# Optimization experiments

Measured on AMD Instinct MI355X. Metric: run time of the kernel, lower is better.

Reference implementation:

```python
import jax, jax.numpy as jnp
import numpy as np

B, IN, OUT, ORDER = 8192, 1024, 1024, 7


def setup_inputs() -> dict:
    key = jax.random.key(0)
    k1, k2 = jax.random.split(key)
    x = jax.random.normal(k1, (B, IN), dtype=jnp.float32)
    tanh_range = jnp.float32(1.0)
    coef = jax.random.normal(k2, (OUT, IN, ORDER + 1), dtype=jnp.float32) * 0.1
    return {"x": x, "tanh_range": tanh_range, "coef": coef}


def _poly(x, tanh_range, order):
    # t^0, t^1, ..., t^order via cumulative products (matches torch recurrence)
    t = jnp.tanh(x * tanh_range)                      # [B, IN]
    powers = jnp.cumprod(jnp.broadcast_to(t[..., None], t.shape + (order,)), axis=-1)
    ones = jnp.ones_like(t)[..., None]
    return jnp.concatenate([ones, powers], axis=-1)   # [B, IN, order+1]


def reference(x, tanh_range, coef):
    poly = _poly(x, tanh_range, ORDER)                # [B, IN, K]
    # output[b, j] = sum_{i,k} coef[j,i,k] * poly[b,i,k]
    return jnp.einsum('bik,jik->bj', poly, coef)
```

## Files before the change

kernel.cpp:

```cpp
#include <hip/hip_runtime.h>
#include <hip/hip_bf16.h>


#define BM 128
#define BN 128
#define BK 64
#define KT 7168
#define KFULL 8192

typedef short bf16x8 __attribute__((ext_vector_type(8)));
typedef short bf16x4 __attribute__((ext_vector_type(4)));
typedef float f32x4  __attribute__((ext_vector_type(4)));

__device__ __forceinline__ unsigned short f2bf(float f) {
    union { float f; unsigned u; } v; v.f = f;
    unsigned r = v.u + 0x7fffu + ((v.u >> 16) & 1u);
    return (unsigned short)(r >> 16);
}

__device__ __forceinline__ void gload_lds16(const void* gp, void* lp) {
    __builtin_amdgcn_global_load_lds(
        (const __attribute__((address_space(1))) void*)gp,
        (__attribute__((address_space(3))) void*)lp, 16, 0, 0);
}

#define CVT_BLOCKS  512
#define TANH_BLOCKS 4096

__global__ __launch_bounds__(256)
void prep(const float* __restrict__ x, const float* __restrict__ trp,
          const float* __restrict__ coef, unsigned short* __restrict__ coef_bf,
          unsigned short* __restrict__ A) {
    const int b = blockIdx.x;
    unsigned short tmp[56];
    if (b < CVT_BLOCKS) {
        const size_t g = (size_t)b * 256 + threadIdx.x;
        const float* src = coef + g * 64;
        float buf[64];
        #pragma unroll
        for (int v = 0; v < 16; ++v) {
            const float4 f = *(const float4*)(src + v * 4);
            buf[v*4+0] = f.x; buf[v*4+1] = f.y; buf[v*4+2] = f.z; buf[v*4+3] = f.w;
        }
        #pragma unroll
        for (int p = 0; p < 8; ++p)
            #pragma unroll
            for (int k = 1; k < 8; ++k)
                tmp[p * 7 + k - 1] = f2bf(buf[p * 8 + k]);
        bf16x8* dst = (bf16x8*)(coef_bf + g * 56);
        #pragma unroll
        for (int v = 0; v < 7; ++v) {
            bf16x8 pk;
            #pragma unroll
            for (int s = 0; s < 8; ++s) pk[s] = (short)tmp[v * 8 + s];
            dst[v] = pk;
        }
    } else {
        const size_t g = (size_t)(b - CVT_BLOCKS) * 256 + threadIdx.x;
        const float tr = trp[0];
        const float4 x0 = *(const float4*)(x + g * 8);
        const float4 x1 = *(const float4*)(x + g * 8 + 4);
        const float xs[8] = {x0.x, x0.y, x0.z, x0.w, x1.x, x1.y, x1.z, x1.w};
        #pragma unroll
        for (int p = 0; p < 8; ++p) {
            const float e  = __expf(2.0f * tr * xs[p]);
            const float tt = 1.0f - 2.0f * __builtin_amdgcn_rcpf(e + 1.0f);
            float pw = tt;
            #pragma unroll
            for (int k = 1; k < 8; ++k) { tmp[p * 7 + k - 1] = f2bf(pw); pw *= tt; }
        }
        bf16x8* dst = (bf16x8*)(A + g * 56);
        #pragma unroll
        for (int v = 0; v < 7; ++v) {
            bf16x8 pk;
            #pragma unroll
            for (int s = 0; s < 8; ++s) pk[s] = (short)tmp[v * 8 + s];
            dst[v] = pk;
        }
    }
}

__global__ __launch_bounds__(256)
void bias_k(const float* __restrict__ coef, float* __restrict__ bias) {
    const int j = blockIdx.x;
    float s = 0.f;
    for (int ii = threadIdx.x; ii < 1024; ii += 256)
        s += coef[(size_t)j * KFULL + (size_t)ii * 8];
    #pragma unroll
    for (int off = 32; off > 0; off >>= 1) s += __shfl_down(s, off, 64);
    __shared__ float ls[4];
    if ((threadIdx.x & 63) == 0) ls[threadIdx.x >> 6] = s;
    __syncthreads();
    if (threadIdx.x == 0) bias[j] = ls[0] + ls[1] + ls[2] + ls[3];
}

__global__ __launch_bounds__(256, 2)
void gemm_bt(const unsigned short* __restrict__ A, const unsigned short* __restrict__ Bt,
             const float* __restrict__ bias, float* __restrict__ out)
{
    __shared__ unsigned short As[BM * BK];
    __shared__ unsigned short Bs[BN * BK];

    const int t    = threadIdx.x;
    const int m0   = blockIdx.x * BM;
    const int n0   = blockIdx.y * BN;
    const int w    = t >> 6;
    const int lane = t & 63;
    const int wm   = (w >> 1) * 64;
    const int wn   = (w & 1) * 64;
    const int lrow = lane & 15;

    const int srow   = t >> 3;
    const int schunk = (t & 7) ^ (srow & 7);
    const int wbase  = w * 512;

    f32x4 acc[4][4];
    #pragma unroll
    for (int i = 0; i < 4; i++)
        #pragma unroll
        for (int j = 0; j < 4; j++)
            acc[i][j] = (f32x4){0.f, 0.f, 0.f, 0.f};

    const size_t abase = (size_t)(m0 + srow) * KT + schunk * 8;
    const size_t bbase = (size_t)(n0 + srow) * KT + schunk * 8;

    for (int k0 = 0; k0 < KT; k0 += BK) {
        #pragma unroll
        for (int r = 0; r < 4; ++r)
            gload_lds16(A + abase + (size_t)r * 32 * KT + k0, &As[r * 2048 + wbase]);
        #pragma unroll
        for (int r = 0; r < 4; ++r)
            gload_lds16(Bt + bbase + (size_t)r * 32 * KT + k0, &Bs[r * 2048 + wbase]);

        __syncthreads();

        #pragma unroll
        for (int kk = 0; kk < BK; kk += 32) {
            const int soff = ((((kk >> 3) + (lane >> 4)) ^ (lane & 7)) * 8);
            bf16x8 a[4], b[4];
            #pragma unroll
            for (int i = 0; i < 4; i++)
                a[i] = *(const bf16x8*)&As[(wm + i * 16 + lrow) * BK + soff];
            #pragma unroll
            for (int j = 0; j < 4; j++)
                b[j] = *(const bf16x8*)&Bs[(wn + j * 16 + lrow) * BK + soff];
            #pragma unroll
            for (int i = 0; i < 4; i++)
                #pragma unroll
                for (int j = 0; j < 4; j++)
                    acc[i][j] = __builtin_amdgcn_mfma_f32_16x16x32_bf16(a[i], b[j], acc[i][j], 0, 0, 0);
        }

        __syncthreads();
    }

    const int crow = (lane >> 4) * 4;
    const int ccol = lane & 15;
    #pragma unroll
    for (int j = 0; j < 4; j++) {
        const int n = n0 + wn + j * 16 + ccol;
        const float bv = bias[n];
        #pragma unroll
        for (int i = 0; i < 4; i++) {
            const int m = m0 + wm + i * 16 + crow;
            #pragma unroll
            for (int r = 0; r < 4; ++r)
                out[(size_t)(m + r) * 1024 + n] = acc[i][j][r] + bv;
        }
    }
}

#define LDK 72
__global__ __launch_bounds__(256, 2)
void taylor_gemm(const float* __restrict__ x, const float* __restrict__ trp,
                 const float* __restrict__ coef, float* __restrict__ out)
{
    __shared__ unsigned short As[BM * LDK];
    __shared__ unsigned short Bs[BN * LDK];

    const int t  = threadIdx.x;
    const int m0 = blockIdx.x * BM;
    const int n0 = blockIdx.y * BN;
    const float tr = trp[0];

    const int w    = t >> 6;
    const int lane = t & 63;
    const int wm   = (w >> 1) * 64;
    const int wn   = (w & 1) * 64;
    const int lrow = lane & 15;
    const int kq   = (lane >> 4) * 8;

    f32x4 acc[4][4];
    #pragma unroll
    for (int i = 0; i < 4; i++)
        #pragma unroll
        for (int j = 0; j < 4; j++)
            acc[i][j] = (f32x4){0.f, 0.f, 0.f, 0.f};

    const int bcol  = t & 15;
    const int brow0 = t >> 4;
    const int acol  = t & 7;
    const int arow0 = t >> 3;

    for (int k0 = 0; k0 < KFULL; k0 += BK) {
        const int i0 = k0 >> 3;
        #pragma unroll
        for (int r = 0; r < 8; ++r) {
            const int row = brow0 + r * 16;
            const float4 v = *(const float4*)(coef + (size_t)(n0 + row) * KFULL + k0 + bcol * 4);
            bf16x4 pk;
            pk[0] = (short)f2bf(v.x); pk[1] = (short)f2bf(v.y);
            pk[2] = (short)f2bf(v.z); pk[3] = (short)f2bf(v.w);
            *(bf16x4*)&Bs[row * LDK + bcol * 4] = pk;
        }
        #pragma unroll
        for (int r = 0; r < 4; ++r) {
            const int row = arow0 + r * 32;
            const float xv = x[(size_t)(m0 + row) * 1024 + i0 + acol];
            const float e  = __expf(2.0f * tr * xv);
            const float tt = 1.0f - 2.0f / (e + 1.0f);
            bf16x8 pk;
            float p = 1.0f;
            #pragma unroll
            for (int k = 0; k < 8; ++k) { pk[k] = (short)f2bf(p); p *= tt; }
            *(bf16x8*)&As[row * LDK + acol * 8] = pk;
        }
        __syncthreads();
        #pragma unroll
        for (int kk = 0; kk < BK; kk += 32) {
            bf16x8 a[4], b[4];
            #pragma unroll
            for (int i = 0; i < 4; i++)
                a[i] = *(const bf16x8*)&As[(wm + i * 16 + lrow) * LDK + kk + kq];
            #pragma unroll
            for (int j = 0; j < 4; j++)
                b[j] = *(const bf16x8*)&Bs[(wn + j * 16 + lrow) * LDK + kk + kq];
            #pragma unroll
            for (int i = 0; i < 4; i++)
                #pragma unroll
                for (int j = 0; j < 4; j++)
                    acc[i][j] = __builtin_amdgcn_mfma_f32_16x16x32_bf16(a[i], b[j], acc[i][j], 0, 0, 0);
        }
        __syncthreads();
    }

    const int crow = (lane >> 4) * 4;
    const int ccol = lane & 15;
    #pragma unroll
    for (int i = 0; i < 4; i++) {
        #pragma unroll
        for (int j = 0; j < 4; j++) {
            const int m = m0 + wm + i * 16 + crow;
            const int n = n0 + wn + j * 16 + ccol;
            #pragma unroll
            for (int r = 0; r < 4; ++r)
                out[(size_t)(m + r) * 1024 + n] = acc[i][j][r];
        }
    }
}

extern "C" void kernel_launch(void* const* d_in, const int* in_sizes, int n_in,
                              void* d_out, int out_size, void* d_ws, size_t ws_size,
                              hipStream_t stream) {
    const float* x    = (const float*)d_in[0];
    const float* trp  = (const float*)d_in[1];
    const float* coef = (const float*)d_in[2];
    float* out = (float*)d_out;

    const size_t A_BYTES    = (size_t)8192 * KT * 2;
    const size_t COEF_BYTES = (size_t)1024 * KT * 2;
    const size_t BIAS_BYTES = 1024 * sizeof(float);
    dim3 block(256);

    if (ws_size >= A_BYTES + COEF_BYTES + BIAS_BYTES) {
        unsigned short* A_bf    = (unsigned short*)d_ws;
        unsigned short* coef_bf = (unsigned short*)((char*)d_ws + A_BYTES);
        float*          bias    = (float*)((char*)d_ws + A_BYTES + COEF_BYTES);

        prep<<<dim3(CVT_BLOCKS + TANH_BLOCKS), block, 0, stream>>>(
            x, trp, coef, coef_bf, A_bf);
        bias_k<<<dim3(1024), block, 0, stream>>>(coef, bias);
        gemm_bt<<<dim3(8192 / BM, 1024 / BN), block, 0, stream>>>(
            A_bf, coef_bf, bias, out);
    } else {
        taylor_gemm<<<dim3(8192 / BM, 1024 / BN), block, 0, stream>>>(x, trp, coef, out);
    }
}
```

Measured before the change: 265.0 us.

## Store bf16 operands in k-chunk-major layout for the GEMM

Changes the intermediate A and coefficient matrices from row-major [rows, K] to a chunked layout [K/8][rows][8], where each 16-byte k-chunk of consecutive rows is contiguous. The prep kernel now writes this layout, and the GEMM loads index it directly. Each row-tile load then touches contiguous 16-byte segments across rows instead of strided rows, which changes global-load coalescing and how each load spreads across memory channels. The prep kernel's writes become strided per thread, and its coef reads are now gathered per output row.

```diff
diff --git a/kernel.cpp b/kernel.cpp
--- a/kernel.cpp
+++ b/kernel.cpp
@@ -31,51 +31,51 @@
 void prep(const float* __restrict__ x, const float* __restrict__ trp,
           const float* __restrict__ coef, unsigned short* __restrict__ coef_bf,
           unsigned short* __restrict__ A) {
-    const int b = blockIdx.x;
+    const int blk = blockIdx.x;
     unsigned short tmp[56];
-    if (b < CVT_BLOCKS) {
-        const size_t g = (size_t)b * 256 + threadIdx.x;
-        const float* src = coef + g * 64;
-        float buf[64];
-        #pragma unroll
-        for (int v = 0; v < 16; ++v) {
-            const float4 f = *(const float4*)(src + v * 4);
-            buf[v*4+0] = f.x; buf[v*4+1] = f.y; buf[v*4+2] = f.z; buf[v*4+3] = f.w;
-        }
-        #pragma unroll
-        for (int p = 0; p < 8; ++p)
-            #pragma unroll
-            for (int k = 1; k < 8; ++k)
-                tmp[p * 7 + k - 1] = f2bf(buf[p * 8 + k]);
-        bf16x8* dst = (bf16x8*)(coef_bf + g * 56);
+    if (blk < CVT_BLOCKS) {
+        const int g  = blk * 256 + threadIdx.x;
+        const int j  = g & 1023;
+        const int ig = g >> 10;
+        const float* src = coef + (size_t)j * KFULL + ig * 64;
+        #pragma unroll
+        for (int i = 0; i < 8; ++i) {
+            const float4 f0 = *(const float4*)(src + i * 8);
+            const float4 f1 = *(const float4*)(src + i * 8 + 4);
+            tmp[i*7+0] = f2bf(f0.y); tmp[i*7+1] = f2bf(f0.z); tmp[i*7+2] = f2bf(f0.w);
+            tmp[i*7+3] = f2bf(f1.x); tmp[i*7+4] = f2bf(f1.y);
+            tmp[i*7+5] = f2bf(f1.z); tmp[i*7+6] = f2bf(f1.w);
+        }
         #pragma unroll
         for (int v = 0; v < 7; ++v) {
             bf16x8 pk;
             #pragma unroll
             for (int s = 0; s < 8; ++s) pk[s] = (short)tmp[v * 8 + s];
-            dst[v] = pk;
+            *(bf16x8*)(coef_bf + ((size_t)(ig * 7 + v) * 1024 + j) * 8) = pk;
         }
     } else {
-        const size_t g = (size_t)(b - CVT_BLOCKS) * 256 + threadIdx.x;
+        const int g  = (blk - CVT_BLOCKS) * 256 + threadIdx.x;
+        const int bb = g & 8191;
+        const int ig = g >> 13;
         const float tr = trp[0];
-        const float4 x0 = *(const float4*)(x + g * 8);
-        const float4 x1 = *(const float4*)(x + g * 8 + 4);
+        const float* xp = x + (size_t)bb * 1024 + ig * 8;
+        const float4 x0 = *(const float4*)xp;
+        const float4 x1 = *(const float4*)(xp + 4);
         const float xs[8] = {x0.x, x0.y, x0.z, x0.w, x1.x, x1.y, x1.z, x1.w};
         #pragma unroll
-        for (int p = 0; p < 8; ++p) {
-            const float e  = __expf(2.0f * tr * xs[p]);
+        for (int i = 0; i < 8; ++i) {
+            const float e  = __expf(2.0f * tr * xs[i]);
             const float tt = 1.0f - 2.0f * __builtin_amdgcn_rcpf(e + 1.0f);
             float pw = tt;
             #pragma unroll
-            for (int k = 1; k < 8; ++k) { tmp[p * 7 + k - 1] = f2bf(pw); pw *= tt; }
-        }
-        bf16x8* dst = (bf16x8*)(A + g * 56);
+            for (int k = 1; k < 8; ++k) { tmp[i * 7 + k - 1] = f2bf(pw); pw *= tt; }
+        }
         #pragma unroll
         for (int v = 0; v < 7; ++v) {
             bf16x8 pk;
             #pragma unroll
             for (int s = 0; s < 8; ++s) pk[s] = (short)tmp[v * 8 + s];
-            dst[v] = pk;
+            *(bf16x8*)(A + ((size_t)(ig * 7 + v) * 8192 + bb) * 8) = pk;
         }
     }
 }
@@ -121,16 +121,18 @@
         for (int j = 0; j < 4; j++)
             acc[i][j] = (f32x4){0.f, 0.f, 0.f, 0.f};
 
-    const size_t abase = (size_t)(m0 + srow) * KT + schunk * 8;
-    const size_t bbase = (size_t)(n0 + srow) * KT + schunk * 8;
+    const size_t aoff = ((size_t)schunk * 8192 + m0 + srow) * 8;
+    const size_t boff = ((size_t)schunk * 1024 + n0 + srow) * 8;
 
     for (int k0 = 0; k0 < KT; k0 += BK) {
+        const unsigned short* ap = A  + aoff + (size_t)(k0 >> 3) * 65536;
+        const unsigned short* bp = Bt + boff + (size_t)(k0 >> 3) * 8192;
         #pragma unroll
         for (int r = 0; r < 4; ++r)
-            gload_lds16(A + abase + (size_t)r * 32 * KT + k0, &As[r * 2048 + wbase]);
+            gload_lds16(ap + r * 256, &As[r * 2048 + wbase]);
         #pragma unroll
         for (int r = 0; r < 4; ++r)
-            gload_lds16(Bt + bbase + (size_t)r * 32 * KT + k0, &Bs[r * 2048 + wbase]);
+            gload_lds16(bp + r * 256, &Bs[r * 2048 + wbase]);
 
         __syncthreads();
 
```

Result: slower. 335.2 us (+26.5%).
